# Performance work log

Hardware: AMD Instinct MI355X
Metric: run time of the kernel (lower is better)

Reference implementation:

```python
import jax, jax.numpy as jnp
import numpy as np

OUT_FEATURES = 11008
IN_FEATURES = 4096
GROUP_SIZE = 32
NUM_GROUPS = OUT_FEATURES * IN_FEATURES // GROUP_SIZE        # 1,409,024
NUM_PACKED = NUM_GROUPS * (GROUP_SIZE // 8 * 3)              # 16,908,288 bytes


def block_dequantize_3bit(weight_q3, weight_norm):
    """Unpack 3-bit codes (8 values per 3 bytes) and dequantize to fp32."""
    p = weight_q3.reshape(-1, 3).astype(jnp.int32)  # [N/8, 3] bytes
    b0, b1, b2 = p[:, 0], p[:, 1], p[:, 2]
    q = jnp.stack([
        b0 & 7,
        (b0 >> 3) & 7,
        ((b0 >> 6) & 3) | ((b1 & 1) << 2),
        (b1 >> 1) & 7,
        (b1 >> 4) & 7,
        ((b1 >> 7) & 1) | ((b2 & 3) << 1),
        (b2 >> 2) & 7,
        (b2 >> 5) & 7,
    ], axis=-1)                                     # [N/8, 8] codes in 0..7
    q = q.reshape(NUM_GROUPS, GROUP_SIZE).astype(jnp.float32)
    norm = weight_norm.astype(jnp.float32)[:, None]  # [num_groups, 1]
    w = (q / 7.0) * 2.0 * norm - norm                # map [0,7] -> [-norm, norm]
    return w.reshape(OUT_FEATURES, IN_FEATURES)


def setup_inputs() -> dict:
    key = jax.random.key(0)
    k1, k2, k3, k4 = jax.random.split(key, 4)
    x = jax.random.normal(k1, (4, 128, IN_FEATURES), dtype=jnp.float32)
    weight_q3 = jax.random.randint(k2, (NUM_PACKED,), 0, 256, dtype=jnp.int32)
    weight_norm = (jax.random.uniform(k3, (NUM_GROUPS,), dtype=jnp.float32) * 0.1 + 0.01).astype(jnp.float16)
    bias = jax.random.normal(k4, (OUT_FEATURES,), dtype=jnp.float32) * 0.02
    return {"x": x, "weight_q3": weight_q3, "weight_norm": weight_norm, "bias": bias}


def reference(x, weight_q3, weight_norm, bias):
    w = block_dequantize_3bit(weight_q3, weight_norm)  # [out, in] fp32
    return jnp.einsum('bsd,od->bso', x, w) + bias
```

## Files before the change

### kernel.cpp

```cpp
#include <hip/hip_runtime.h>
#include <hip/hip_fp16.h>

#define M_TOTAL 512
#define N_TOTAL 11008
#define K_TOTAL 4096
#define BM 128
#define BN 64
#define BK 64
#define NT (K_TOTAL / BK)
#define LDK 72

typedef short bf16x8 __attribute__((ext_vector_type(8)));
typedef _Float16 fp16x8 __attribute__((ext_vector_type(8)));
typedef float f32x4 __attribute__((ext_vector_type(4)));

__device__ __forceinline__ unsigned int pack2_bf16(float f0, float f1) {
    unsigned int u0 = __builtin_bit_cast(unsigned int, f0) + 0x8000u;
    unsigned int u1 = __builtin_bit_cast(unsigned int, f1) + 0x8000u;
    return (u0 >> 16) | (u1 & 0xFFFF0000u);
}

__device__ __forceinline__ void async_ld16(void* lds, const void* g) {
    __builtin_amdgcn_global_load_lds(
        (const __attribute__((address_space(1))) unsigned int*)g,
        (__attribute__((address_space(3))) unsigned int*)lds, 16, 0, 0);
}

__device__ __forceinline__ int detect_mode_wave(const void* __restrict__ wn) {
    const int lane = threadIdx.x & 63;
    const unsigned short* u16 = (const unsigned short*)wn;
    const float* f32p = (const float*)wn;
    const float vb = __builtin_bit_cast(float, (unsigned int)u16[lane] << 16);
    const float vh = __half2float(__builtin_bit_cast(__half, u16[lane]));
    const float vf = f32p[lane];
    const unsigned long long mb = __ballot(vb > 0.005f && vb < 0.12f);
    const unsigned long long mh = __ballot(vh > 0.005f && vh < 0.12f);
    (void)vf;
    return (mb == ~0ull) ? 2 : ((mh == ~0ull) ? 1 : 0);
}

__global__ void __launch_bounds__(256)
convert_x_kernel(const float* __restrict__ x, unsigned short* __restrict__ xb) {
    const int i = (blockIdx.x * 256 + threadIdx.x) * 4;
    const float4 v = *(const float4*)&x[i];
    const __half2 p0 = __floats2half2_rn(v.x, v.y);
    const __half2 p1 = __floats2half2_rn(v.z, v.w);
    *(uint2*)&xb[i] = make_uint2(__builtin_bit_cast(unsigned int, p0),
                                 __builtin_bit_cast(unsigned int, p1));
}

__global__ void __launch_bounds__(256, 3)
l3b_gemm_pipe(const unsigned short* __restrict__ xb, const int* __restrict__ wq,
              const void* __restrict__ wnorm, const float* __restrict__ bias,
              float* __restrict__ out)
{
    __shared__ unsigned short As[2][BM * 64];
    __shared__ unsigned short Bs[2][BN * 64];

    const int tid  = threadIdx.x;
    const int mode = detect_mode_wave(wnorm);

    const int bid = blockIdx.x;
    const int w   = (bid & 7) * 86 + (bid >> 3);
    const int m0  = (w & 3) * BM;
    const int n0  = (w >> 2) * BN;

    const int wid  = tid >> 6;
    const int lane = tid & 63;
    const int quad = lane >> 4;
    const int lm   = lane & 15;
    const int wm   = (wid >> 1) * 64;
    const int wn_  = (wid & 1) * 32;

    const int arow0 = wid * 8 + (lane >> 3);
    const int acol  = ((lane & 7) ^ ((lane >> 3) & 7)) * 8;
    const int aslot = (lane & 7) * 8;

    const int gl   = tid >> 1;
    const int hf   = tid & 1;
    const int bn_l = gl >> 1;
    const int kg   = gl & 1;
    const int sw   = bn_l & 7;
    const int c0   = kg * 4 + hf * 2;
    const int ldsB0 = (bn_l << 6) + (((c0    ) ^ sw) << 3);
    const int ldsB1 = (bn_l << 6) + (((c0 + 1) ^ sw) << 3);

    auto stageA = [&](int it, int buf) {
#pragma unroll
        for (int j = 0; j < 4; ++j) {
            const int row = arow0 + j * 32;
            async_ld16(&As[buf][(row << 6) + aslot],
                       &xb[(size_t)(m0 + row) * K_TOTAL + it * 64 + acol]);
        }
    };

    auto loadNorm = [&](int g) -> float {
        if (mode == 0)      return ((const float*)wnorm)[g];
        else if (mode == 1) return __half2float(((const __half*)wnorm)[g]);
        else                return __builtin_bit_cast(float,
                               (unsigned int)((const unsigned short*)wnorm)[g] << 16);
    };
    auto loadB = [&](int it, int2& w0, int2& w1, int2& w2, float& nrm) {
        const int g    = (n0 + bn_l) * (K_TOTAL / 32) + it * 2 + kg;
        const int base = g * 12 + hf * 6;
        w0 = *(const int2*)&wq[base];
        w1 = *(const int2*)&wq[base + 2];
        w2 = *(const int2*)&wq[base + 4];
        nrm = loadNorm(g);
    };
    auto decodeB = [&](int2 w0, int2 w1, int2 w2, float nrm, int buf) {
        const float af = nrm * (16.0f / 7.0f);
        const float bf = nrm * (-23.0f / 7.0f);
        const __half2 A2 = __float2half2_rn(af);
        const __half2 B2 = __float2half2_rn(bf);
        const unsigned int bits0 =
            (unsigned)w0.x | ((unsigned)w0.y << 8) | ((unsigned)w1.x << 16);
        const unsigned int bits1 =
            (unsigned)w1.y | ((unsigned)w2.x << 8) | ((unsigned)w2.y << 16);
        unsigned int packs[8];
#pragma unroll
        for (int t3 = 0; t3 < 2; ++t3) {
            const unsigned int bits = t3 ? bits1 : bits0;
#pragma unroll
            for (int j = 0; j < 4; ++j) {
                const unsigned int q0 = (bits >> (6 * j)) & 7u;
                const unsigned int q1 = (bits >> (6 * j + 3)) & 7u;
                const unsigned int y  = 0x3C003C00u | (q0 << 7) | (q1 << 23);
                const __half2 wv = __hfma2(__builtin_bit_cast(__half2, y), A2, B2);
                packs[t3 * 4 + j] = __builtin_bit_cast(unsigned int, wv);
            }
        }
        *(uint4*)&Bs[buf][ldsB0] = make_uint4(packs[0], packs[1], packs[2], packs[3]);
        *(uint4*)&Bs[buf][ldsB1] = make_uint4(packs[4], packs[5], packs[6], packs[7]);
    };

    f32x4 acc[4][2];
#pragma unroll
    for (int i = 0; i < 4; ++i)
#pragma unroll
        for (int j = 0; j < 2; ++j) acc[i][j] = (f32x4){0.f, 0.f, 0.f, 0.f};

    auto mfmaTile = [&](const unsigned short* Asb, const unsigned short* Bsb) {
#pragma unroll
        for (int ks = 0; ks < 2; ++ks) {
            const int cswz = (((ks * 4 + quad) ^ (lm & 7)) << 3);
            fp16x8 aF[4], bF[2];
#pragma unroll
            for (int mi = 0; mi < 4; ++mi)
                aF[mi] = *(const fp16x8*)&Asb[((wm + mi * 16 + lm) << 6) + cswz];
#pragma unroll
            for (int ni = 0; ni < 2; ++ni)
                bF[ni] = *(const fp16x8*)&Bsb[((wn_ + ni * 16 + lm) << 6) + cswz];
            __builtin_amdgcn_s_setprio(1);
#pragma unroll
            for (int mi = 0; mi < 4; ++mi)
#pragma unroll
                for (int ni = 0; ni < 2; ++ni)
                    acc[mi][ni] = __builtin_amdgcn_mfma_f32_16x16x32_f16(
                        aF[mi], bF[ni], acc[mi][ni], 0, 0, 0);
            __builtin_amdgcn_s_setprio(0);
        }
    };

    int2 w0a, w1a, w2a; float na;
    int2 w0b, w1b, w2b; float nb;

    stageA(0, 0);
    loadB(0, w0a, w1a, w2a, na);
    decodeB(w0a, w1a, w2a, na, 0);
    loadB(1, w0b, w1b, w2b, nb);
    __syncthreads();

    for (int it = 0; it < NT; it += 2) {
        if (it + 1 < NT) stageA(it + 1, 1);
        __builtin_amdgcn_sched_barrier(0);
        if (it + 2 < NT) loadB(it + 2, w0a, w1a, w2a, na);
        if (it + 1 < NT) decodeB(w0b, w1b, w2b, nb, 1);
        mfmaTile(As[0], Bs[0]);
        if (it + 2 < NT) {
            asm volatile("s_waitcnt vmcnt(3) lgkmcnt(0)" ::: "memory");
        } else {
            asm volatile("s_waitcnt vmcnt(0) lgkmcnt(0)" ::: "memory");
        }
        __builtin_amdgcn_s_barrier();

        if (it + 2 < NT) stageA(it + 2, 0);
        __builtin_amdgcn_sched_barrier(0);
        if (it + 3 < NT) loadB(it + 3, w0b, w1b, w2b, nb);
        if (it + 2 < NT) decodeB(w0a, w1a, w2a, na, 0);
        mfmaTile(As[1], Bs[1]);
        if (it + 3 < NT) {
            asm volatile("s_waitcnt vmcnt(3) lgkmcnt(0)" ::: "memory");
        } else {
            asm volatile("s_waitcnt vmcnt(0) lgkmcnt(0)" ::: "memory");
        }
        __builtin_amdgcn_s_barrier();
    }

#pragma unroll
    for (int ni = 0; ni < 2; ++ni) {
        const int o  = n0 + wn_ + ni * 16 + lm;
        const float bv = bias[o];
#pragma unroll
        for (int mi = 0; mi < 4; ++mi) {
#pragma unroll
            for (int r = 0; r < 4; ++r) {
                const int m = m0 + wm + mi * 16 + quad * 4 + r;
                out[m * N_TOTAL + o] = acc[mi][ni][r] + bv;
            }
        }
    }
}

__global__ void __launch_bounds__(256)
l3b_gemm_kernel(const float* __restrict__ x, const int* __restrict__ wq,
                const void* __restrict__ wnorm, const float* __restrict__ bias,
                float* __restrict__ out)
{
    __shared__ unsigned short As[128 * LDK];
    __shared__ unsigned short Bs[64 * LDK];

    const int mode = detect_mode_wave(wnorm);
    const int tid  = threadIdx.x;
    const int m0   = blockIdx.y * 128;
    const int n0   = blockIdx.x * 64;
    const int wid  = tid >> 6;
    const int lane = tid & 63;
    const int quad = lane >> 4;
    const int lm   = lane & 15;
    const int wm   = (wid >> 1) * 64;
    const int wn   = (wid & 1) * 32;

    f32x4 acc[4][2];
#pragma unroll
    for (int i = 0; i < 4; ++i)
#pragma unroll
        for (int j = 0; j < 2; ++j) acc[i][j] = (f32x4){0.f, 0.f, 0.f, 0.f};

    const int ar = tid >> 4;
    const int ac = (tid & 15) * 4;
    const int gin      = tid >> 1;
    const int half     = tid & 1;
    const int bn_local = gin >> 1;
    const int bkg      = gin & 1;

    for (int it = 0; it < NT; ++it) {
        const int k0 = it * BK;
        __syncthreads();
#pragma unroll
        for (int p = 0; p < 8; ++p) {
            const int row = p * 16 + ar;
            const float4 v = *(const float4*)&x[(m0 + row) * K_TOTAL + k0 + ac];
            *(uint2*)&As[row * LDK + ac] =
                make_uint2(pack2_bf16(v.x, v.y), pack2_bf16(v.z, v.w));
        }
        {
            const int g    = (n0 + bn_local) * (K_TOTAL / 32) + it * 2 + bkg;
            const int base = g * 12 + half * 6;
            const int2 w0 = *(const int2*)&wq[base];
            const int2 w1 = *(const int2*)&wq[base + 2];
            const int2 w2 = *(const int2*)&wq[base + 4];
            float nrm;
            if (mode == 0)      nrm = ((const float*)wnorm)[g];
            else if (mode == 1) nrm = __half2float(((const __half*)wnorm)[g]);
            else                nrm = __builtin_bit_cast(float,
                                    (unsigned int)((const unsigned short*)wnorm)[g] << 16);
            const float a = nrm * (2.0f / 7.0f);
            const float b = -nrm;
            const unsigned int bits0 =
                (unsigned)w0.x | ((unsigned)w0.y << 8) | ((unsigned)w1.x << 16);
            const unsigned int bits1 =
                (unsigned)w1.y | ((unsigned)w2.x << 8) | ((unsigned)w2.y << 16);
            unsigned int packs[8];
#pragma unroll
            for (int t3 = 0; t3 < 2; ++t3) {
                const unsigned int bits = t3 ? bits1 : bits0;
#pragma unroll
                for (int j = 0; j < 4; ++j) {
                    const float f0 = fmaf((float)((bits >> (6 * j)) & 7), a, b);
                    const float f1 = fmaf((float)((bits >> (6 * j + 3)) & 7), a, b);
                    packs[t3 * 4 + j] = pack2_bf16(f0, f1);
                }
            }
            unsigned int* dst = (unsigned int*)&Bs[bn_local * LDK + bkg * 32 + half * 16];
            *(uint4*)dst       = make_uint4(packs[0], packs[1], packs[2], packs[3]);
            *(uint4*)(dst + 4) = make_uint4(packs[4], packs[5], packs[6], packs[7]);
        }
        __syncthreads();
#pragma unroll
        for (int ks = 0; ks < 2; ++ks) {
            const int kb = ks * 32 + quad * 8;
            bf16x8 aF[4], bF[2];
#pragma unroll
            for (int mi = 0; mi < 4; ++mi)
                aF[mi] = *(const bf16x8*)&As[(wm + mi * 16 + lm) * LDK + kb];
#pragma unroll
            for (int ni = 0; ni < 2; ++ni)
                bF[ni] = *(const bf16x8*)&Bs[(wn + ni * 16 + lm) * LDK + kb];
#pragma unroll
            for (int mi = 0; mi < 4; ++mi)
#pragma unroll
                for (int ni = 0; ni < 2; ++ni)
                    acc[mi][ni] = __builtin_amdgcn_mfma_f32_16x16x32_bf16(
                        aF[mi], bF[ni], acc[mi][ni], 0, 0, 0);
        }
    }
#pragma unroll
    for (int ni = 0; ni < 2; ++ni) {
        const int o  = n0 + wn + ni * 16 + lm;
        const float bv = bias[o];
#pragma unroll
        for (int mi = 0; mi < 4; ++mi)
#pragma unroll
            for (int r = 0; r < 4; ++r) {
                const int m = m0 + wm + mi * 16 + quad * 4 + r;
                out[m * N_TOTAL + o] = acc[mi][ni][r] + bv;
            }
    }
}

extern "C" void kernel_launch(void* const* d_in, const int* in_sizes, int n_in,
                              void* d_out, int out_size, void* d_ws, size_t ws_size,
                              hipStream_t stream) {
    const float* x    = (const float*)d_in[0];
    const int*   wq   = (const int*)d_in[1];
    const void*  wn   = d_in[2];
    const float* bias = (const float*)d_in[3];
    float* out = (float*)d_out;

    const size_t need = 256 + (size_t)M_TOTAL * K_TOTAL * 2;
    if (ws_size >= need) {
        unsigned short* xb = (unsigned short*)((char*)d_ws + 256);
        convert_x_kernel<<<(M_TOTAL * K_TOTAL / 4) / 256, 256, 0, stream>>>(x, xb);
        l3b_gemm_pipe<<<(M_TOTAL / BM) * (N_TOTAL / BN), 256, 0, stream>>>(
            xb, wq, wn, bias, out);
    } else {
        dim3 grid(N_TOTAL / 64, M_TOTAL / 128);
        l3b_gemm_kernel<<<grid, 256, 0, stream>>>(x, wq, wn, bias, out);
    }
}
```

Before: 199.2 us.

## Decode 3-bit weights directly into MFMA B-fragment registers, dropping B LDS staging

```diff
diff --git a/kernel.cpp b/kernel.cpp
--- a/kernel.cpp
+++ b/kernel.cpp
@@ -55,7 +55,6 @@
               float* __restrict__ out)
 {
     __shared__ unsigned short As[2][BM * 64];
-    __shared__ unsigned short Bs[2][BN * 64];
 
     const int tid  = threadIdx.x;
     const int mode = detect_mode_wave(wnorm);
@@ -76,15 +75,6 @@
     const int acol  = ((lane & 7) ^ ((lane >> 3) & 7)) * 8;
     const int aslot = (lane & 7) * 8;
 
-    const int gl   = tid >> 1;
-    const int hf   = tid & 1;
-    const int bn_l = gl >> 1;
-    const int kg   = gl & 1;
-    const int sw   = bn_l & 7;
-    const int c0   = kg * 4 + hf * 2;
-    const int ldsB0 = (bn_l << 6) + (((c0    ) ^ sw) << 3);
-    const int ldsB1 = (bn_l << 6) + (((c0 + 1) ^ sw) << 3);
-
     auto stageA = [&](int it, int buf) {
 #pragma unroll
         for (int j = 0; j < 4; ++j) {
@@ -100,101 +90,105 @@
         else                return __builtin_bit_cast(float,
                                (unsigned int)((const unsigned short*)wnorm)[g] << 16);
     };
-    auto loadB = [&](int it, int2& w0, int2& w1, int2& w2, float& nrm) {
-        const int g    = (n0 + bn_l) * (K_TOTAL / 32) + it * 2 + kg;
-        const int base = g * 12 + hf * 6;
-        w0 = *(const int2*)&wq[base];
-        w1 = *(const int2*)&wq[base + 2];
-        w2 = *(const int2*)&wq[base + 4];
-        nrm = loadNorm(g);
-    };
-    auto decodeB = [&](int2 w0, int2 w1, int2 w2, float nrm, int buf) {
-        const float af = nrm * (16.0f / 7.0f);
-        const float bf = nrm * (-23.0f / 7.0f);
-        const __half2 A2 = __float2half2_rn(af);
-        const __half2 B2 = __float2half2_rn(bf);
-        const unsigned int bits0 =
-            (unsigned)w0.x | ((unsigned)w0.y << 8) | ((unsigned)w1.x << 16);
-        const unsigned int bits1 =
-            (unsigned)w1.y | ((unsigned)w2.x << 8) | ((unsigned)w2.y << 16);
-        unsigned int packs[8];
-#pragma unroll
-        for (int t3 = 0; t3 < 2; ++t3) {
-            const unsigned int bits = t3 ? bits1 : bits0;
-#pragma unroll
-            for (int j = 0; j < 4; ++j) {
-                const unsigned int q0 = (bits >> (6 * j)) & 7u;
-                const unsigned int q1 = (bits >> (6 * j + 3)) & 7u;
-                const unsigned int y  = 0x3C003C00u | (q0 << 7) | (q1 << 23);
-                const __half2 wv = __hfma2(__builtin_bit_cast(__half2, y), A2, B2);
-                packs[t3 * 4 + j] = __builtin_bit_cast(unsigned int, wv);
-            }
-        }
-        *(uint4*)&Bs[buf][ldsB0] = make_uint4(packs[0], packs[1], packs[2], packs[3]);
-        *(uint4*)&Bs[buf][ldsB1] = make_uint4(packs[4], packs[5], packs[6], packs[7]);
+
+    struct BP { int b0[4], b1[4], b2[4]; float nrm[4]; };
+    struct BF { fp16x8 f[4]; };
+
+    auto loadBP = [&](int it, BP& P) {
+#pragma unroll
+        for (int u = 0; u < 4; ++u) {
+            const int ks = u >> 1, ni = u & 1;
+            const int c  = n0 + wn_ + ni * 16 + lm;
+            const int g  = c * (K_TOTAL / 32) + it * 2 + ks;
+            const int base = g * 12 + quad * 3;
+            P.b0[u] = wq[base];
+            P.b1[u] = wq[base + 1];
+            P.b2[u] = wq[base + 2];
+            P.nrm[u] = loadNorm(g);
+        }
+    };
+
+    auto decodeBF = [&](int b0, int b1, int b2, float nrm) -> fp16x8 {
+        const __half2 A2 = __float2half2_rn(nrm * (16.0f / 7.0f));
+        const __half2 B2 = __float2half2_rn(nrm * (-23.0f / 7.0f));
+        const unsigned int bits =
+            (unsigned)b0 | ((unsigned)b1 << 8) | ((unsigned)b2 << 16);
+        union { unsigned int u[4]; fp16x8 v; } r;
+#pragma unroll
+        for (int j = 0; j < 4; ++j) {
+            const unsigned int q0 = (bits >> (6 * j)) & 7u;
+            const unsigned int q1 = (bits >> (6 * j + 3)) & 7u;
+            const unsigned int y  = 0x3C003C00u | (q0 << 7) | (q1 << 23);
+            r.u[j] = __builtin_bit_cast(unsigned int,
+                       __hfma2(__builtin_bit_cast(__half2, y), A2, B2));
+        }
+        return r.v;
+    };
+
+    auto decodeAll = [&](const BP& P, BF& F) {
+#pragma unroll
+        for (int u = 0; u < 4; ++u)
+            F.f[u] = decodeBF(P.b0[u], P.b1[u], P.b2[u], P.nrm[u]);
     };
 
     f32x4 acc[4][2];
 #pragma unroll
-    for (int i = 0; i < 4; ++i)
-#pragma unroll
-        for (int j = 0; j < 2; ++j) acc[i][j] = (f32x4){0.f, 0.f, 0.f, 0.f};
-
-    auto mfmaTile = [&](const unsigned short* Asb, const unsigned short* Bsb) {
+    for (int i = 0; i < 2; ++i)
+#pragma unroll
+        for (int j = 0; j < 2; ++j) { acc[i][j] = (f32x4){0.f,0.f,0.f,0.f};
+                                      acc[i+2][j] = (f32x4){0.f,0.f,0.f,0.f}; }
+
+    auto mfmaStep = [&](const unsigned short* Asb, const BF& F) {
 #pragma unroll
         for (int ks = 0; ks < 2; ++ks) {
             const int cswz = (((ks * 4 + quad) ^ (lm & 7)) << 3);
-            fp16x8 aF[4], bF[2];
+            fp16x8 aF[4];
 #pragma unroll
             for (int mi = 0; mi < 4; ++mi)
                 aF[mi] = *(const fp16x8*)&Asb[((wm + mi * 16 + lm) << 6) + cswz];
 #pragma unroll
-            for (int ni = 0; ni < 2; ++ni)
-                bF[ni] = *(const fp16x8*)&Bsb[((wn_ + ni * 16 + lm) << 6) + cswz];
-            __builtin_amdgcn_s_setprio(1);
-#pragma unroll
-            for (int mi = 0; mi < 4; ++mi)
-#pragma unroll
-                for (int ni = 0; ni < 2; ++ni)
+            for (int ni = 0; ni < 2; ++ni) {
+                __builtin_amdgcn_s_setprio(1);
+#pragma unroll
+                for (int mi = 0; mi < 4; ++mi)
                     acc[mi][ni] = __builtin_amdgcn_mfma_f32_16x16x32_f16(
-                        aF[mi], bF[ni], acc[mi][ni], 0, 0, 0);
-            __builtin_amdgcn_s_setprio(0);
-        }
-    };
-
-    int2 w0a, w1a, w2a; float na;
-    int2 w0b, w1b, w2b; float nb;
+                        aF[mi], F.f[ks * 2 + ni], acc[mi][ni], 0, 0, 0);
+                __builtin_amdgcn_s_setprio(0);
+            }
+        }
+    };
+
+    BP P;
+    BF Fa, Fb;
 
     stageA(0, 0);
-    loadB(0, w0a, w1a, w2a, na);
-    decodeB(w0a, w1a, w2a, na, 0);
-    loadB(1, w0b, w1b, w2b, nb);
+    loadBP(0, P);
+    asm volatile("s_waitcnt vmcnt(0)" ::: "memory");
+    decodeAll(P, Fa);
     __syncthreads();
 
     for (int it = 0; it < NT; it += 2) {
-        if (it + 1 < NT) stageA(it + 1, 1);
-        __builtin_amdgcn_sched_barrier(0);
-        if (it + 2 < NT) loadB(it + 2, w0a, w1a, w2a, na);
-        if (it + 1 < NT) decodeB(w0b, w1b, w2b, nb, 1);
-        mfmaTile(As[0], Bs[0]);
+        stageA(it + 1, 1);
+        loadBP(it + 1, P);
+        __builtin_amdgcn_sched_barrier(0);
+        mfmaStep(As[0], Fa);
+        __builtin_amdgcn_sched_barrier(0);
+        asm volatile("s_waitcnt vmcnt(0)" ::: "memory");
+        decodeAll(P, Fb);
+        __builtin_amdgcn_s_barrier();
+        __builtin_amdgcn_sched_barrier(0);
+
         if (it + 2 < NT) {
-            asm volatile("s_waitcnt vmcnt(3) lgkmcnt(0)" ::: "memory");
-        } else {
-            asm volatile("s_waitcnt vmcnt(0) lgkmcnt(0)" ::: "memory");
-        }
+            stageA(it + 2, 0);
+            loadBP(it + 2, P);
+        }
+        __builtin_amdgcn_sched_barrier(0);
+        mfmaStep(As[1], Fb);
+        __builtin_amdgcn_sched_barrier(0);
+        asm volatile("s_waitcnt vmcnt(0)" ::: "memory");
+        if (it + 2 < NT) decodeAll(P, Fa);
         __builtin_amdgcn_s_barrier();
-
-        if (it + 2 < NT) stageA(it + 2, 0);
-        __builtin_amdgcn_sched_barrier(0);
-        if (it + 3 < NT) loadB(it + 3, w0b, w1b, w2b, nb);
-        if (it + 2 < NT) decodeB(w0a, w1a, w2a, na, 0);
-        mfmaTile(As[1], Bs[1]);
-        if (it + 3 < NT) {
-            asm volatile("s_waitcnt vmcnt(3) lgkmcnt(0)" ::: "memory");
-        } else {
-            asm volatile("s_waitcnt vmcnt(0) lgkmcnt(0)" ::: "memory");
-        }
-        __builtin_amdgcn_s_barrier();
+        __builtin_amdgcn_sched_barrier(0);
     }
 
 #pragma unroll
```

Result: slower. 317.5 us (+59.4%).
